# Performance work log

Hardware: AMD Instinct MI355X
Metric: run time of the kernel (lower is better)

The kernel has to match this reference:

```python
import jax, jax.numpy as jnp
import numpy as np
from jax import lax

ORDER = 6
WN = 0.5 / 50.0          # highpass_cutoff / (orig_fs/2)
UP, DOWN = 16, 25        # 64/100 reduced by gcd 4 (scipy resample_poly)
HALF_LEN = 10 * DOWN     # scipy kaiser half length = 10*max_rate
NTAPS = 2 * HALF_LEN + 1
PADLEN = 21              # sosfiltfilt default: 3*(2*n_sections+1), 3 biquads
CHANNELS = np.array([126, 125, 48, 112, 67, 93, 10, 61, 39, 108])
D_MODEL = 16
LN_EPS = 1e-5


def _butter_hp_sos(order, wn):
    # scipy.signal.butter(order, wn, btype='high', output='sos') in pure numpy
    fs = 2.0
    warped = 2.0 * fs * np.tan(np.pi * wn / fs)
    m = np.arange(-order + 1, order, 2)
    p = -np.exp(1j * np.pi * m / (2 * order))     # analog LP prototype poles
    k = np.real(1.0 / np.prod(-p))                # lp2hp gain (no zeros)
    p = warped / p                                # lp2hp poles; zeros at s=0
    z = np.zeros(order)
    fs2 = 2.0 * fs                                # bilinear, fs=2
    k = k * np.real(np.prod(fs2 - z) / np.prod(fs2 - p))
    z = (fs2 + z) / (fs2 - z)                     # digital zeros, all +1
    p = (fs2 + p) / (fs2 - p)
    pp = p[np.imag(p) > 0]
    pp = pp[np.argsort(-np.abs(np.abs(pp) - 1.0))]  # closest to unit circle last
    sos = []
    for i, pi in enumerate(pp):
        b = np.array([1.0, -2.0, 1.0]) * (k if i == 0 else 1.0)
        a = np.array([1.0, -2.0 * pi.real, np.abs(pi) ** 2])
        sos.append(np.concatenate([b, a]))
    return np.array(sos)


def _sosfilt_zi(sos):
    # scipy.signal.sosfilt_zi: steady-state of step response per section
    n = sos.shape[0]
    zi = np.zeros((n, 2))
    scale = 1.0
    for s in range(n):
        b0, b1, b2, _, a1, a2 = sos[s]
        A = np.array([[1.0 + a1, -1.0], [a2, 1.0]])
        B = np.array([b1 - a1 * b0, b2 - a2 * b0])
        zi[s] = scale * np.linalg.solve(A, B)
        scale *= (b0 + b1 + b2) / (1.0 + a1 + a2)
    return zi


SOS = _butter_hp_sos(ORDER, WN)
ZI = _sosfilt_zi(SOS)


def _resample_fir():
    # scipy firwin(2*half_len+1, 1/max_rate, window=('kaiser',5.0)) * up
    fc = 1.0 / DOWN
    m = np.arange(NTAPS) - (NTAPS - 1) / 2.0
    h = fc * np.sinc(fc * m) * np.kaiser(NTAPS, 5.0)
    h /= h.sum()
    return h * UP


H_BASE = _resample_fir()


def _pos_encoding(max_len, d):
    pos = np.arange(max_len)[:, None].astype(np.float64)
    div = np.exp(np.arange(0, d, 2) * (-np.log(10000.0) / d))
    pe = np.zeros((max_len, d))
    pe[:, 0::2] = np.sin(pos * div)
    pe[:, 1::2] = np.cos(pos * div)
    return pe.astype(np.float32)


PE = _pos_encoding(3840, D_MODEL)


def _sosfilt(x, zi):
    # x: (N,T), zi: (N,3,2). Cascade of biquads, transposed direct form II.
    sos = jnp.asarray(SOS, x.dtype)
    nsec = SOS.shape[0]

    def step(z, xt):
        v = xt
        zs = []
        for s in range(nsec):  # fixed tiny cascade, unrolled inside scan
            b0, b1, b2, a1, a2 = sos[s, 0], sos[s, 1], sos[s, 2], sos[s, 4], sos[s, 5]
            y = b0 * v + z[s][0]
            zs.append((b1 * v - a1 * y + z[s][1], b2 * v - a2 * y))
            v = y
        return tuple(zs), v

    z0 = tuple((zi[:, s, 0], zi[:, s, 1]) for s in range(nsec))
    _, y = lax.scan(step, z0, x.T)
    return y.T


def _sosfiltfilt(x):
    # scipy.signal.sosfiltfilt with default odd padding, padlen=21
    zi = jnp.asarray(ZI, x.dtype)
    front = 2.0 * x[:, :1] - x[:, PADLEN:0:-1]
    back = 2.0 * x[:, -1:] - x[:, -2:-PADLEN - 2:-1]
    ext = jnp.concatenate([front, x, back], axis=1)
    y = _sosfilt(ext, zi[None] * ext[:, 0, None, None])
    y = y[:, ::-1]
    y = _sosfilt(y, zi[None] * y[:, 0, None, None])
    return y[:, ::-1][:, PADLEN:-PADLEN]


def _resample_poly(x):
    # scipy.signal.resample_poly(x, 64, 100): upfirdn via dilated conv
    T = x.shape[-1]
    n_out = (T * UP) // DOWN + int((T * UP) % DOWN != 0)
    n_pre_pad = DOWN - HALF_LEN % DOWN
    n_pre_remove = (HALF_LEN + n_pre_pad) // DOWN

    def outlen(lh):
        return (((T - 1) * UP + lh) - 1) // DOWN + 1

    n_post = 0
    while outlen(NTAPS + n_pre_pad + n_post) < n_out + n_pre_remove:
        n_post += 1
    h = np.concatenate([np.zeros(n_pre_pad), H_BASE, np.zeros(n_post)])
    L = h.size
    rhs = jnp.asarray(h[::-1].copy(), x.dtype).reshape(1, 1, L)
    y = lax.conv_general_dilated(x[:, None, :], rhs, window_strides=(DOWN,),
                                 padding=[(L - 1, L - 1)], lhs_dilation=(UP,),
                                 dimension_numbers=('NCH', 'OIH', 'NCH'))
    return y[:, 0, n_pre_remove:n_pre_remove + n_out]


def _ln(x, g, b):
    mu = x.mean(-1, keepdims=True)
    var = ((x - mu) ** 2).mean(-1, keepdims=True)
    return (x - mu) * lax.rsqrt(var + LN_EPS) * g + b


def setup_inputs() -> dict:
    key = jax.random.key(0)
    ks = jax.random.split(key, 20)
    f32 = jnp.float32
    d = {
        'x': jax.random.normal(ks[0], (64, 128, 2000), f32),
        'conv_w': jax.random.normal(ks[1], (16, 10, 3), f32) * 0.15,
        'conv_b': jnp.zeros((16,), f32),
        'ln0_g': jnp.ones((16,), f32), 'ln0_b': jnp.zeros((16,), f32),
        'wqkv': jax.random.normal(ks[2], (48, 16), f32) * 0.125,
        'bqkv': jnp.zeros((48,), f32),
        'wo': jax.random.normal(ks[3], (16, 16), f32) * 0.25,
        'bo': jnp.zeros((16,), f32),
        'w1': jax.random.normal(ks[4], (32, 16), f32) * 0.2,
        'b1': jnp.zeros((32,), f32),
        'w2': jax.random.normal(ks[5], (16, 32), f32) * 0.2,
        'b2': jnp.zeros((16,), f32),
        'ln1_g': jnp.ones((16,), f32), 'ln1_b': jnp.zeros((16,), f32),
        'ln2_g': jnp.ones((16,), f32), 'ln2_b': jnp.zeros((16,), f32),
        'wfc': jax.random.normal(ks[6], (1, 16), f32) * 0.3,
        'bfc': jnp.zeros((1,), f32),
    }
    return d


def reference(x, conv_w, conv_b, ln0_g, ln0_b, wqkv, bqkv, wo, bo,
              w1, b1, w2, b2, ln1_g, ln1_b, ln2_g, ln2_b, wfc, bfc):
    B = x.shape[0]
    # remove Cz (last channel) then gather interesting channels
    x = x[:, :-1, :][:, jnp.asarray(CHANNELS), :]        # (B,10,T)
    x = x - x.mean(axis=1, keepdims=True)                # CAR
    C, T = x.shape[1], x.shape[2]
    xf = _sosfiltfilt(x.reshape(B * C, T))               # zero-phase highpass
    xr = _resample_poly(xf)                              # 100 Hz -> 64 Hz
    x = xr.reshape(B, C, -1)
    x = jnp.tanh(x)                                      # artifact_scale = 1.0
    mean = x.mean(axis=2, keepdims=True)                 # zscore, unbiased std
    var = ((x - mean) ** 2).sum(axis=2, keepdims=True) / (x.shape[2] - 1)
    std = jnp.maximum(jnp.sqrt(var), 1e-6)
    x = (x - mean) / std
    # conv1d k=3 pad=1 (10 -> 16) + relu
    x = lax.conv_general_dilated(x, conv_w, (1,), [(1, 1)],
                                 dimension_numbers=('NCH', 'OIH', 'NCH'))
    x = jax.nn.relu(x + conv_b[None, :, None])
    x = x.transpose(0, 2, 1)                             # (B,S,16)
    x = _ln(x, ln0_g, ln0_b)
    x = x + jnp.asarray(PE[:x.shape[1]], x.dtype)[None]
    # TransformerEncoderLayer, post-norm, nhead=1, relu FFN (eval: no dropout)
    qkv = x @ wqkv.T + bqkv
    q, k, v = jnp.split(qkv, 3, axis=-1)
    att = jax.nn.softmax(jnp.einsum('bqd,bkd->bqk', q, k) * 0.25, axis=-1)
    a = jnp.einsum('bqk,bkd->bqd', att, v) @ wo.T + bo
    x = _ln(x + a, ln1_g, ln1_b)
    f = jax.nn.relu(x @ w1.T + b1) @ w2.T + b2
    x = _ln(x + f, ln2_g, ln2_b)
    pooled = x.mean(axis=1)                              # adaptive avg pool -> 1
    return pooled @ wfc.T + bfc                          # (B,1)
```

## Files before the change

### kernel.cpp

```cpp
#include <hip/hip_runtime.h>
#include <cmath>
#include <complex>
#include <algorithm>

#ifndef M_PI
#define M_PI 3.14159265358979323846
#endif

typedef _Float16 f16x8 __attribute__((ext_vector_type(8)));
typedef _Float16 f16x4 __attribute__((ext_vector_type(4)));
typedef __fp16 fp16x2 __attribute__((ext_vector_type(2)));
typedef float f32x4 __attribute__((ext_vector_type(4)));

struct FiltArg {
  double b0[3], b1[3], b2[3], a1[3], a2[3];
  double zi0[3], zi1[3];
};
struct CorArg { double CA[16 * 6]; };
struct EigArg {
  double Pm[36], Pinv[36];
  double czi[6];
  double lam_re[3], lam_im[3];
  double lami_re[3], lami_im[3];
};
struct FirArg { float h[526]; };

static void design_sos(FiltArg& sa) {
  const int order = 6;
  const double wn = 0.5 / 50.0;
  const double fs = 2.0;
  double warped = 2.0 * fs * std::tan(M_PI * wn / fs);
  std::complex<double> p[6];
  for (int i = 0; i < order; i++) {
    int m = -order + 1 + 2 * i;
    p[i] = -std::exp(std::complex<double>(0.0, M_PI * m / (2.0 * order)));
  }
  std::complex<double> prod1(1, 0);
  for (int i = 0; i < 6; i++) prod1 *= -p[i];
  double k = (1.0 / prod1).real();
  for (int i = 0; i < 6; i++) p[i] = warped / p[i];
  const double fs2 = 2.0 * fs;
  std::complex<double> num(1, 0), den(1, 0);
  for (int i = 0; i < 6; i++) { num *= fs2; den *= (fs2 - p[i]); }
  k *= (num / den).real();
  for (int i = 0; i < 6; i++) p[i] = (fs2 + p[i]) / (fs2 - p[i]);
  std::complex<double> pp[3]; int n = 0;
  for (int i = 0; i < 6; i++) if (p[i].imag() > 0) pp[n++] = p[i];
  std::stable_sort(pp, pp + 3,
    [](const std::complex<double>& A, const std::complex<double>& B) {
      return std::fabs(std::abs(A) - 1.0) > std::fabs(std::abs(B) - 1.0);
    });
  double sos[3][6];
  for (int s = 0; s < 3; s++) {
    double g = (s == 0) ? k : 1.0;
    sos[s][0] = g; sos[s][1] = -2.0 * g; sos[s][2] = g;
    sos[s][3] = 1.0; sos[s][4] = -2.0 * pp[s].real(); sos[s][5] = std::norm(pp[s]);
  }
  double scale = 1.0;
  for (int s = 0; s < 3; s++) {
    double b0 = sos[s][0], b1 = sos[s][1], b2 = sos[s][2];
    double a1 = sos[s][4], a2 = sos[s][5];
    double det = 1.0 + a1 + a2;
    double r0 = b1 - a1 * b0, r1 = b2 - a2 * b0;
    double z0 = (r0 + r1) / det;
    double z1 = ((1.0 + a1) * r1 - a2 * r0) / det;
    sa.b0[s] = b0; sa.b1[s] = b1; sa.b2[s] = b2; sa.a1[s] = a1; sa.a2[s] = a2;
    sa.zi0[s] = scale * z0; sa.zi1[s] = scale * z1;
    scale *= (b0 + b1 + b2) / (1.0 + a1 + a2);
  }
}

static double host_step(const FiltArg& c, double z[6], double v) {
  for (int s = 0; s < 3; s++) {
    double y = c.b0[s] * v + z[2 * s];
    z[2 * s]     = c.b1[s] * v - c.a1[s] * y + z[2 * s + 1];
    z[2 * s + 1] = c.b2[s] * v - c.a2[s] * y;
    v = y;
  }
  return v;
}

static void build_filt(FiltArg& c, CorArg& co) {
  design_sos(c);
  for (int j = 0; j < 6; j++) {
    double z[6] = {0, 0, 0, 0, 0, 0};
    z[j] = 1.0;
    for (int i = 0; i < 16; i++) co.CA[i * 6 + j] = host_step(c, z, 0.0);
  }
}

static void build_eig(const FiltArg& c, EigArg& e) {
  double Pr[36];
  for (int s = 0; s < 3; s++) {
    double a1 = c.a1[s], a2 = c.a2[s];
    std::complex<double> disc = std::sqrt(std::complex<double>(a1 * a1 - 4.0 * a2, 0.0));
    std::complex<double> p = (-a1 + disc) / 2.0;
    if (p.imag() < 0) p = std::conj(p);
    std::complex<double> v[6] = {0, 0, 0, 0, 0, 0};
    v[2 * s] = 1.0;
    v[2 * s + 1] = a1 + p;
    std::complex<double> y = 1.0;
    for (int j = s + 1; j < 3; j++) {
      double b0j = c.b0[j], b1j = c.b1[j], b2j = c.b2[j];
      double a1j = c.a1[j], a2j = c.a2[j];
      std::complex<double> det = p * p + a1j * p + a2j;
      std::complex<double> r0 = (b1j - a1j * b0j) * y;
      std::complex<double> r1 = (b2j - a2j * b0j) * y;
      std::complex<double> z0 = (p * r0 + r1) / det;
      std::complex<double> z1 = ((p + a1j) * r1 - a2j * r0) / det;
      v[2 * j] = z0; v[2 * j + 1] = z1;
      y = b0j * y + z0;
    }
    for (int i = 0; i < 6; i++) {
      Pr[i * 6 + 2 * s]     = v[i].real();
      Pr[i * 6 + 2 * s + 1] = v[i].imag();
    }
    std::complex<double> lam = std::pow(p, 16);
    e.lam_re[s] = lam.real(); e.lam_im[s] = lam.imag();
    std::complex<double> li = 1.0 / lam;
    e.lami_re[s] = li.real(); e.lami_im[s] = li.imag();
  }
  for (int i = 0; i < 36; i++) e.Pm[i] = Pr[i];
  double M[6][12];
  for (int i = 0; i < 6; i++)
    for (int j = 0; j < 6; j++) { M[i][j] = Pr[i * 6 + j]; M[i][6 + j] = (i == j) ? 1.0 : 0.0; }
  for (int col = 0; col < 6; col++) {
    int piv = col;
    for (int i = col + 1; i < 6; i++)
      if (std::fabs(M[i][col]) > std::fabs(M[piv][col])) piv = i;
    if (piv != col) for (int j = 0; j < 12; j++) std::swap(M[col][j], M[piv][j]);
    double d = M[col][col];
    for (int j = 0; j < 12; j++) M[col][j] /= d;
    for (int i = 0; i < 6; i++) if (i != col) {
      double f = M[i][col];
      for (int j = 0; j < 12; j++) M[i][j] -= f * M[col][j];
    }
  }
  for (int i = 0; i < 6; i++)
    for (int j = 0; j < 6; j++) e.Pinv[i * 6 + j] = M[i][6 + j];
  double zv[6];
  for (int s = 0; s < 3; s++) { zv[2 * s] = c.zi0[s]; zv[2 * s + 1] = c.zi1[s]; }
  for (int i = 0; i < 6; i++) {
    double sum = 0.0;
    for (int j = 0; j < 6; j++) sum += e.Pinv[i * 6 + j] * zv[j];
    e.czi[i] = sum;
  }
}

static double bessel_i0(double x) {
  double s = 1.0, t = 1.0;
  for (int k = 1; k < 64; k++) {
    double u = x / (2.0 * k);
    t *= u * u; s += t;
    if (t < 1e-18 * s) break;
  }
  return s;
}

static void design_fir(FirArg& fa) {
  double h[501];
  const double fc = 1.0 / 25.0;
  double denom = bessel_i0(5.0);
  double sum = 0.0;
  for (int nn = 0; nn < 501; nn++) {
    double m = nn - 250.0;
    double xx = fc * m;
    double snc = (nn == 250) ? 1.0 : std::sin(M_PI * xx) / (M_PI * xx);
    double r = (2.0 * nn) / 500.0 - 1.0;
    double w = bessel_i0(5.0 * std::sqrt(std::max(0.0, 1.0 - r * r))) / denom;
    h[nn] = fc * snc * w; sum += h[nn];
  }
  for (int nn = 0; nn < 25; nn++) fa.h[nn] = 0.0f;
  for (int nn = 0; nn < 501; nn++) fa.h[25 + nn] = (float)(h[nn] / sum * 16.0);
}

__device__ inline double waveReduceSum(double v) {
  #pragma unroll
  for (int off = 32; off > 0; off >>= 1) v += __shfl_down(v, off, 64);
  return v;
}

__device__ inline void cpow_int(double br, double bi, int n, double& rr_, double& ri_) {
  double rr = 1.0, ri = 0.0;
  while (n) {
    if (n & 1) { double t = rr * br - ri * bi; ri = rr * bi + ri * br; rr = t; }
    double t2 = br * br - bi * bi; bi = 2.0 * br * bi; br = t2;
    n >>= 1;
  }
  rr_ = rr; ri_ = ri;
}

#define XR(t) xr[(t) + ((t) >> 5)]
#define YF(t) yf[(t) + ((t) >> 5)]
__global__ __launch_bounds__(128) void k_filt_resamp(const float* __restrict__ xin,
                                                     float* __restrict__ xn,
                                                     float* __restrict__ pe,
                                                     float* __restrict__ out,
                                                     FiltArg c, CorArg co, EigArg eg,
                                                     FirArg fa) {
  int bid = blockIdx.x;
  int gk = threadIdx.x;
  if (bid >= 640) {
    int i = (bid - 640) * 128 + gk;
    int t = i >> 4, d = i & 15, j2 = d >> 1;
    double div = exp(-((double)(2 * j2)) * 0.5756462732485114);
    double a = (double)t * div;
    pe[i] = (float)((d & 1) ? cos(a) : sin(a));
    if (bid == 799 && gk < 64) out[gk] = 0.f;
    return;
  }
  int r = (bid & 7) * 80 + (bid >> 3);
  __shared__ float xd[2000];
  __shared__ float xr[2112];
  __shared__ double yf[2112];
  __shared__ double wsum[3][2];
  __shared__ float hl[526];
  __shared__ double red[4];
  int lane = gk & 63;
  int wv = gk >> 6;
  int bb = r / 10, cc = r % 10;
  const int ch[10] = {126, 125, 48, 112, 67, 93, 10, 61, 39, 108};
  const float* xb = xin + (size_t)bb * 128 * 2000;

  for (int i = gk; i < 526; i += 128) hl[i] = fa.h[i];
  for (int t = gk; t < 2000; t += 128) {
    float own = 0.f, ssum = 0.f;
    #pragma unroll
    for (int c2 = 0; c2 < 10; c2++) {
      float vv = xb[ch[c2] * 2000 + t];
      ssum += vv;
      if (c2 == cc) own = vv;
    }
    xd[t] = own - ssum * 0.1f;
  }
  __syncthreads();

  float x0f = xd[0], xlf = xd[1999];
  for (int t = gk; t < 2048; t += 128) {
    float v;
    if (t < 21)        v = 2.f * x0f - xd[21 - t];
    else if (t < 2021) v = xd[t - 21];
    else if (t < 2042) v = 2.f * xlf - xd[4019 - t];
    else               v = 0.f;
    XR(t) = v;
  }
  __syncthreads();

  double b0[3], b1[3], b2[3], a1[3], a2[3];
  #pragma unroll
  for (int s = 0; s < 3; s++) {
    b0[s] = c.b0[s]; b1[s] = c.b1[s]; b2[s] = c.b2[s];
    a1[s] = c.a1[s]; a2[s] = c.a2[s];
  }
  auto step = [&](double* z, double v) -> double {
    #pragma unroll
    for (int s = 0; s < 3; s++) {
      double y = b0[s] * v + z[2 * s];
      z[2 * s]     = b1[s] * v - a1[s] * y + z[2 * s + 1];
      z[2 * s + 1] = b2[s] * v - a2[s] * y;
      v = y;
    }
    return v;
  };

  auto eigscan = [&](double seed, const double* F, double* zst) {
    double G[6];
    #pragma unroll
    for (int i = 0; i < 6; i++) {
      double s = 0.0;
      #pragma unroll
      for (int j = 0; j < 6; j++) s += eg.Pinv[i * 6 + j] * F[j];
      G[i] = s;
    }
    double tre[3], tim[3], sre[3], sim[3];
    #pragma unroll
    for (int s3 = 0; s3 < 3; s3++) {
      double gre = G[2 * s3], gim = -G[2 * s3 + 1];
      double mre, mim;
      cpow_int(eg.lami_re[s3], eg.lami_im[s3], gk, mre, mim);
      tre[s3] = mre * gre - mim * gim;
      tim[s3] = mre * gim + mim * gre;
      double pr = tre[s3], pi = tim[s3];
      #pragma unroll
      for (int off = 1; off < 64; off <<= 1) {
        double ore = __shfl_up(pr, off, 64);
        double oim = __shfl_up(pi, off, 64);
        pr += (lane >= off) ? ore : 0.0;
        pi += (lane >= off) ? oim : 0.0;
      }
      sre[s3] = pr; sim[s3] = pi;
      if (wv == 0 && lane == 63) { wsum[s3][0] = pr; wsum[s3][1] = pi; }
    }
    __syncthreads();
    double coord[6];
    #pragma unroll
    for (int s3 = 0; s3 < 3; s3++) {
      double inc_re = sre[s3] + (wv ? wsum[s3][0] : 0.0);
      double inc_im = sim[s3] + (wv ? wsum[s3][1] : 0.0);
      double Sre = inc_re - tre[s3], Sim = inc_im - tim[s3];
      double c0re = seed * eg.czi[2 * s3];
      double c0im = -seed * eg.czi[2 * s3 + 1];
      double lkre, lkim;
      cpow_int(eg.lam_re[s3], eg.lam_im[s3], gk, lkre, lkim);
      double lm1re = lkre * eg.lami_re[s3] - lkim * eg.lami_im[s3];
      double lm1im = lkre * eg.lami_im[s3] + lkim * eg.lami_re[s3];
      if (gk == 0) { lm1re = 0.0; lm1im = 0.0; }
      double cre = lkre * c0re - lkim * c0im + lm1re * Sre - lm1im * Sim;
      double cim = lkre * c0im + lkim * c0re + lm1re * Sim + lm1im * Sre;
      coord[2 * s3] = cre;
      coord[2 * s3 + 1] = -cim;
    }
    #pragma unroll
    for (int i = 0; i < 6; i++) {
      double s = 0.0;
      #pragma unroll
      for (int j = 0; j < 6; j++) s += eg.Pm[i * 6 + j] * coord[j];
      zst[i] = s;
    }
  };

  int t0 = gk * 16;
  double z[6], yreg[16], zst[6];

  #pragma unroll
  for (int i = 0; i < 6; i++) z[i] = 0.0;
  for (int i = 0; i < 16; i++) yreg[i] = step(z, (double)XR(t0 + i));
  eigscan((double)XR(0), z, zst);
  for (int i = 0; i < 16; i++) {
    double corr = 0.0;
    #pragma unroll
    for (int j = 0; j < 6; j++) corr += co.CA[i * 6 + j] * zst[j];
    YF(t0 + i) = yreg[i] + corr;
  }
  __syncthreads();

  auto rin = [&](int j) -> double { return (j <= 2041) ? YF(2041 - j) : 0.0; };
  double seedB = YF(2041);
  #pragma unroll
  for (int i = 0; i < 6; i++) z[i] = 0.0;
  for (int i = 0; i < 16; i++) yreg[i] = step(z, rin(t0 + i));
  eigscan(seedB, z, zst);
  for (int i = 0; i < 16; i++) {
    int j = t0 + i;
    if (j >= 21 && j <= 2020) {
      double corr = 0.0;
      #pragma unroll
      for (int jj = 0; jj < 6; jj++) corr += co.CA[i * 6 + jj] * zst[jj];
      xd[2020 - j] = (float)(yreg[i] + corr);
    }
  }
  __syncthreads();

  float vals[10];
  #pragma unroll
  for (int kk = 0; kk < 10; kk++) {
    int o = gk + kk * 128;
    int P = 25 * (o + 11);
    int phase = P & 15;
    float acc = 0.f;
    for (int m = phase; m <= 525; m += 16) {
      int idx = (P - m) >> 4;
      if (idx >= 0 && idx < 2000) acc += hl[m] * xd[idx];
    }
    vals[kk] = tanhf(acc);
  }
  double s = 0.0, ss = 0.0;
  #pragma unroll
  for (int kk = 0; kk < 10; kk++) {
    s += (double)vals[kk]; ss += (double)vals[kk] * (double)vals[kk];
  }
  s = waveReduceSum(s); ss = waveReduceSum(ss);
  if (lane == 0) { red[wv] = s; red[2 + wv] = ss; }
  __syncthreads();
  double S = red[0] + red[1];
  double SS = red[2] + red[3];
  double mean = S / 1280.0;
  double var = (SS - 1280.0 * mean * mean) / 1279.0;
  double sd = fmax(sqrt(fmax(var, 0.0)), 1e-6);
  float fmean = (float)mean, finv = (float)(1.0 / sd);
  #pragma unroll
  for (int kk = 0; kk < 10; kk++)
    xn[(size_t)r * 1280 + gk + kk * 128] = (vals[kk] - fmean) * finv;
}

__global__ __launch_bounds__(256) void k_conv_ln_pe_qkv(const float* __restrict__ xn,
    const float* __restrict__ cw, const float* __restrict__ cb,
    const float* __restrict__ g0, const float* __restrict__ bt0,
    const float* __restrict__ wqkv, const float* __restrict__ bqkv,
    const float* __restrict__ pe,
    float* __restrict__ x0, _Float16* __restrict__ Qh,
    _Float16* __restrict__ Kp, _Float16* __restrict__ Vt_g) {
  __shared__ float w[480], bias[16], gg[16], gb[16];
  __shared__ float wq[768], bq[48];
  for (int i = threadIdx.x; i < 480; i += 256) w[i] = cw[i];
  for (int i = threadIdx.x; i < 768; i += 256) wq[i] = wqkv[i];
  if (threadIdx.x < 16) {
    bias[threadIdx.x] = cb[threadIdx.x];
    gg[threadIdx.x] = g0[threadIdx.x];
    gb[threadIdx.x] = bt0[threadIdx.x];
  }
  if (threadIdx.x < 48) bq[threadIdx.x] = bqkv[threadIdx.x];
  __syncthreads();
  int idx = blockIdx.x * 256 + threadIdx.x;
  int b = idx / 1280, t = idx % 1280;
  const float* xb = xn + (size_t)b * 10 * 1280;
  float in[10][3];
  #pragma unroll
  for (int i = 0; i < 10; i++)
    #pragma unroll
    for (int k = 0; k < 3; k++) {
      int tt = t - 1 + k;
      in[i][k] = (tt >= 0 && tt < 1280) ? xb[i * 1280 + tt] : 0.f;
    }
  float o[16];
  #pragma unroll
  for (int oc = 0; oc < 16; oc++) {
    float a = bias[oc];
    #pragma unroll
    for (int i = 0; i < 10; i++)
      #pragma unroll
      for (int k = 0; k < 3; k++) a += in[i][k] * w[oc * 30 + i * 3 + k];
    o[oc] = fmaxf(a, 0.f);
  }
  float mu = 0.f;
  #pragma unroll
  for (int d = 0; d < 16; d++) mu += o[d];
  mu *= (1.f / 16.f);
  float var = 0.f;
  #pragma unroll
  for (int d = 0; d < 16; d++) { float dd = o[d] - mu; var += dd * dd; }
  var *= (1.f / 16.f);
  float inv = 1.f / sqrtf(var + 1e-5f);
  float xv[16];
  float* outp = x0 + (size_t)idx * 16;
  const float* pep = pe + t * 16;
  #pragma unroll
  for (int d = 0; d < 16; d++) {
    xv[d] = (o[d] - mu) * inv * gg[d] + gb[d] + pep[d];
    outp[d] = xv[d];
  }
  _Float16* qh = Qh + (size_t)idx * 16;
  #pragma unroll
  for (int j = 0; j < 16; j++) {
    float a = bq[j];
    #pragma unroll
    for (int d = 0; d < 16; d++) a += xv[d] * wq[j * 16 + d];
    qh[j] = (_Float16)(0.36067376f * a);
  }
  {
    _Float16* kp = Kp + (size_t)idx * 16;
    #pragma unroll
    for (int j = 0; j < 16; j++) {
      float a = bq[16 + j];
      #pragma unroll
      for (int d = 0; d < 16; d++) a += xv[d] * wq[(16 + j) * 16 + d];
      kp[j] = (_Float16)a;
    }
  }
  {
    _Float16* vt = Vt_g + (size_t)b * 16 * 1280 + t;
    #pragma unroll
    for (int j = 0; j < 16; j++) {
      float a = bq[32 + j];
      #pragma unroll
      for (int d = 0; d < 16; d++) a += xv[d] * wq[(32 + j) * 16 + d];
      vt[j * 1280] = (_Float16)a;
    }
  }
}

#define SHIFT2 17.3123404907f
__global__ __launch_bounds__(256) void k_attn_combine(const _Float16* __restrict__ Qh,
    const _Float16* __restrict__ Kp, const _Float16* __restrict__ Vt_g,
    const float* __restrict__ x0,
    const float* __restrict__ wo, const float* __restrict__ bo,
    const float* __restrict__ w1, const float* __restrict__ b1,
    const float* __restrict__ w2, const float* __restrict__ b2,
    const float* __restrict__ g1, const float* __restrict__ bb1,
    const float* __restrict__ g2, const float* __restrict__ bb2,
    const float* __restrict__ wfc, const float* __restrict__ bfc,
    float* __restrict__ out) {
  __shared__ __align__(16) _Float16 Ks[2][128 * 16];
  __shared__ __align__(16) _Float16 Vt[2][16 * 136];
  __shared__ float Aly[64][17];
  __shared__ float swo[256], sw1[512], sw2[512];
  __shared__ float sbo[16], sb1[32], sb2[16], sg1[16], sbb1[16], sg2[16], sbb2[16];
  __shared__ float swf[16];
  int tid = threadIdx.x;
  int bid = blockIdx.x;
  int jj  = bid >> 3;
  int b   = (bid & 7) + 8 * (jj & 7);
  int rg  = jj >> 3;
  int wv = tid >> 6;
  int lane = tid & 63;
  int col = lane & 15;
  int quad = lane >> 4;
  size_t base = (size_t)b * 1280;
  int row0 = rg * 64 + wv * 16;

  swo[tid] = wo[tid];
  for (int i = tid; i < 512; i += 256) { sw1[i] = w1[i]; sw2[i] = w2[i]; }
  if (tid < 16) {
    sbo[tid] = bo[tid]; sb2[tid] = b2[tid];
    sg1[tid] = g1[tid]; sbb1[tid] = bb1[tid];
    sg2[tid] = g2[tid]; sbb2[tid] = bb2[tid];
    swf[tid] = wfc[tid];
  }
  if (tid < 32) sb1[tid] = b1[tid];

  f16x8 qf;
  #pragma unroll
  for (int j = 0; j < 8; j++) qf[j] = (_Float16)0.f;
  if (quad < 2)
    qf = *(const f16x8*)(Qh + (base + row0 + col) * 16 + quad * 8);

  f16x8 ones;
  #pragma unroll
  for (int j = 0; j < 8; j++) ones[j] = (_Float16)1.f;

  const _Float16* kp_b = Kp + base * 16;
  const _Float16* vt_b = Vt_g + (size_t)b * 16 * 1280;

  int srow = tid >> 1, shalf = tid & 1;
  int sd = tid >> 4, sseg = tid & 15;

  {
    f16x8 kreg = *(const f16x8*)(kp_b + (size_t)srow * 16 + shalf * 8);
    f16x8 vreg = *(const f16x8*)(vt_b + (size_t)sd * 1280 + sseg * 8);
    *(f16x8*)&Ks[0][srow * 16 + shalf * 8] = kreg;
    *(f16x8*)&Vt[0][sd * 136 + sseg * 8] = vreg;
  }

  f32x4 oacc = {0.f, 0.f, 0.f, 0.f};
  f32x4 lacc = {0.f, 0.f, 0.f, 0.f};

  int sA = col + ((quad & 1) ? 32 : 0);
  int sB = sA + 16;
  bool hi = (quad >= 2);

  union U32H2 { fp16x2 h; unsigned int u; };
  union PFU { unsigned int u[4]; f16x8 v; };

  for (int s = 0; s < 10; s++) {
    int cur = s & 1;
    f16x8 kreg, vreg;
    if (s < 9) {
      kreg = *(const f16x8*)(kp_b + (size_t)((s + 1) * 128 + srow) * 16 + shalf * 8);
      vreg = *(const f16x8*)(vt_b + (size_t)sd * 1280 + (s + 1) * 128 + sseg * 8);
    }
    __syncthreads();
    const _Float16* ks = &Ks[cur][0];
    const _Float16* vt = &Vt[cur][0];

    unsigned int pp[8][2];
    #pragma unroll
    for (int st = 0; st < 8; st++) {
      f16x8 af;
      #pragma unroll
      for (int j = 0; j < 8; j++) af[j] = (_Float16)0.f;
      if (quad < 2)
        af = *(const f16x8*)&ks[(st * 16 + col) * 16 + quad * 8];
      f32x4 sf = {-SHIFT2, -SHIFT2, -SHIFT2, -SHIFT2};
      sf = __builtin_amdgcn_mfma_f32_16x16x32_f16(af, qf, sf, 0, 0, 0);
      float e0 = __builtin_amdgcn_exp2f(sf[0]);
      float e1 = __builtin_amdgcn_exp2f(sf[1]);
      float e2 = __builtin_amdgcn_exp2f(sf[2]);
      float e3 = __builtin_amdgcn_exp2f(sf[3]);
      U32H2 t0, t1;
      t0.h = __builtin_amdgcn_cvt_pkrtz(e0, e1);
      t1.h = __builtin_amdgcn_cvt_pkrtz(e2, e3);
      pp[st][0] = t0.u;
      pp[st][1] = t1.u;
    }

    #pragma unroll
    for (int c = 0; c < 4; c++) {
      int a00 = __shfl((int)pp[2 * c][0], sA, 64);
      int a01 = __shfl((int)pp[2 * c][1], sA, 64);
      int a10 = __shfl((int)pp[2 * c + 1][0], sA, 64);
      int a11 = __shfl((int)pp[2 * c + 1][1], sA, 64);
      int b00 = __shfl((int)pp[2 * c][0], sB, 64);
      int b01 = __shfl((int)pp[2 * c][1], sB, 64);
      int b10 = __shfl((int)pp[2 * c + 1][0], sB, 64);
      int b11 = __shfl((int)pp[2 * c + 1][1], sB, 64);
      PFU pu;
      pu.u[0] = (unsigned int)(hi ? a10 : a00);
      pu.u[1] = (unsigned int)(hi ? a11 : a01);
      pu.u[2] = (unsigned int)(hi ? b10 : b00);
      pu.u[3] = (unsigned int)(hi ? b11 : b01);
      f16x8 pf = pu.v;
      f16x8 vf = *(const f16x8*)&vt[col * 136 + c * 32 + quad * 8];
      oacc = __builtin_amdgcn_mfma_f32_16x16x32_f16(pf, vf, oacc, 0, 0, 0);
      lacc = __builtin_amdgcn_mfma_f32_16x16x32_f16(pf, ones, lacc, 0, 0, 0);
    }
    if (s < 9) {
      *(f16x8*)&Ks[cur ^ 1][srow * 16 + shalf * 8] = kreg;
      *(f16x8*)&Vt[cur ^ 1][sd * 136 + sseg * 8] = vreg;
    }
  }

  #pragma unroll
  for (int r = 0; r < 4; r++)
    Aly[wv * 16 + quad * 4 + r][col] = oacc[r] / lacc[r];
  __syncthreads();

  if (tid < 64) {
    int grow = rg * 64 + tid;
    size_t goff = (base + grow) * 16;
    float a[16];
    #pragma unroll
    for (int d = 0; d < 16; d++) a[d] = Aly[tid][d];
    float h[16];
    const float* xr = x0 + goff;
    #pragma unroll
    for (int d = 0; d < 16; d++) {
      float o = sbo[d];
      #pragma unroll
      for (int e = 0; e < 16; e++) o += a[e] * swo[d * 16 + e];
      h[d] = xr[d] + o;
    }
    float mu = 0.f;
    #pragma unroll
    for (int d = 0; d < 16; d++) mu += h[d];
    mu *= (1.f / 16.f);
    float var = 0.f;
    #pragma unroll
    for (int d = 0; d < 16; d++) { float dd = h[d] - mu; var += dd * dd; }
    var *= (1.f / 16.f);
    float inv = 1.f / sqrtf(var + 1e-5f);
    float x1[16];
    #pragma unroll
    for (int d = 0; d < 16; d++) x1[d] = (h[d] - mu) * inv * sg1[d] + sbb1[d];
    float t1[32];
    #pragma unroll
    for (int j = 0; j < 32; j++) {
      float u = sb1[j];
      #pragma unroll
      for (int d = 0; d < 16; d++) u += x1[d] * sw1[j * 16 + d];
      t1[j] = fmaxf(u, 0.f);
    }
    float h2[16];
    #pragma unroll
    for (int d = 0; d < 16; d++) {
      float u = sb2[d];
      #pragma unroll
      for (int j = 0; j < 32; j++) u += t1[j] * sw2[d * 32 + j];
      h2[d] = x1[d] + u;
    }
    mu = 0.f;
    #pragma unroll
    for (int d = 0; d < 16; d++) mu += h2[d];
    mu *= (1.f / 16.f);
    var = 0.f;
    #pragma unroll
    for (int d = 0; d < 16; d++) { float dd = h2[d] - mu; var += dd * dd; }
    var *= (1.f / 16.f);
    inv = 1.f / sqrtf(var + 1e-5f);
    float pv = 0.f;
    #pragma unroll
    for (int d = 0; d < 16; d++)
      pv += ((h2[d] - mu) * inv * sg2[d] + sbb2[d]) * swf[d];
    double part = waveReduceSum((double)pv);
    if (tid == 0) {
      float add = (float)(part / 1280.0);
      if (rg == 0) add += bfc[0];
      atomicAdd(&out[b], add);
    }
  }
}

extern "C" void kernel_launch(void* const* d_in, const int* in_sizes, int n_in,
                              void* d_out, int out_size, void* d_ws, size_t ws_size,
                              hipStream_t stream) {
  const float* x    = (const float*)d_in[0];
  const float* cw   = (const float*)d_in[1];
  const float* cb   = (const float*)d_in[2];
  const float* g0   = (const float*)d_in[3];
  const float* bt0  = (const float*)d_in[4];
  const float* wqkv = (const float*)d_in[5];
  const float* bqkv = (const float*)d_in[6];
  const float* wo   = (const float*)d_in[7];
  const float* bo   = (const float*)d_in[8];
  const float* w1   = (const float*)d_in[9];
  const float* b1   = (const float*)d_in[10];
  const float* w2   = (const float*)d_in[11];
  const float* b2   = (const float*)d_in[12];
  const float* g1   = (const float*)d_in[13];
  const float* bb1  = (const float*)d_in[14];
  const float* g2   = (const float*)d_in[15];
  const float* bb2  = (const float*)d_in[16];
  const float* wfc  = (const float*)d_in[17];
  const float* bfc  = (const float*)d_in[18];
  float* out = (float*)d_out;

  float* ws = (float*)d_ws;
  float* xs = ws;
  float* y1 = xs + 1280000;
  float* xn = y1 + 1306880;
  float* x0 = xn + 819200;
  _Float16* Qh   = (_Float16*)(x0 + 1310720);
  _Float16* Kp   = (_Float16*)(x0 + 1310720 + 655360);
  _Float16* Vt_g = (_Float16*)(x0 + 1310720 + 2 * 655360);
  float* pe = x0 + 1310720 + 3 * 655360;

  FiltArg fc; CorArg co; EigArg eg; FirArg fa;
  build_filt(fc, co);
  build_eig(fc, eg);
  design_fir(fa);

  k_filt_resamp<<<800, 128, 0, stream>>>(x, xn, pe, out, fc, co, eg, fa);
  k_conv_ln_pe_qkv<<<320, 256, 0, stream>>>(xn, cw, cb, g0, bt0, wqkv, bqkv,
                                            pe, x0, Qh, Kp, Vt_g);
  k_attn_combine<<<1280, 256, 0, stream>>>(Qh, Kp, Vt_g, x0, wo, bo, w1, b1,
                                           w2, b2, g1, bb1, g2, bb2, wfc, bfc,
                                           out);
}
```

Baseline: 235.8 us.

## Run the IIR filtfilt scan in fp32 with 256 threads and 8-sample chunks

Moves the biquad cascade, the eigen-decomposed parallel scan and the correction terms from double to float, and stores the intermediate forward-pass signal as float in shared memory. Each block now has 256 threads, each handling 8 samples instead of 16 (the eigenvalue power is updated to match). The cross-wave prefix sum now combines four waves, and the resample/zscore stage uses 5 outputs per thread. This aims to cut fp64 arithmetic and register pressure and to expose more parallelism per block. It risks accuracy loss, because a low-cutoff highpass with poles close to the unit circle is sensitive to single precision.

```diff
diff --git a/kernel.cpp b/kernel.cpp
--- a/kernel.cpp
+++ b/kernel.cpp
@@ -11,6 +11,8 @@
 typedef _Float16 f16x4 __attribute__((ext_vector_type(4)));
 typedef __fp16 fp16x2 __attribute__((ext_vector_type(2)));
 typedef float f32x4 __attribute__((ext_vector_type(4)));
+
+#define CHUNK 8
 
 struct FiltArg {
   double b0[3], b1[3], b2[3], a1[3], a2[3];
@@ -115,7 +117,7 @@
       Pr[i * 6 + 2 * s]     = v[i].real();
       Pr[i * 6 + 2 * s + 1] = v[i].imag();
     }
-    std::complex<double> lam = std::pow(p, 16);
+    std::complex<double> lam = std::pow(p, CHUNK);
     e.lam_re[s] = lam.real(); e.lam_im[s] = lam.imag();
     std::complex<double> li = 1.0 / lam;
     e.lami_re[s] = li.real(); e.lami_im[s] = li.imag();
@@ -180,19 +182,19 @@
   return v;
 }
 
-__device__ inline void cpow_int(double br, double bi, int n, double& rr_, double& ri_) {
-  double rr = 1.0, ri = 0.0;
+__device__ inline void cpowf_int(float br, float bi, int n, float& rr_, float& ri_) {
+  float rr = 1.f, ri = 0.f;
   while (n) {
-    if (n & 1) { double t = rr * br - ri * bi; ri = rr * bi + ri * br; rr = t; }
-    double t2 = br * br - bi * bi; bi = 2.0 * br * bi; br = t2;
+    if (n & 1) { float t = rr * br - ri * bi; ri = rr * bi + ri * br; rr = t; }
+    float t2 = br * br - bi * bi; bi = 2.f * br * bi; br = t2;
     n >>= 1;
   }
   rr_ = rr; ri_ = ri;
 }
 
 #define XR(t) xr[(t) + ((t) >> 5)]
-#define YF(t) yf[(t) + ((t) >> 5)]
-__global__ __launch_bounds__(128) void k_filt_resamp(const float* __restrict__ xin,
+#define YFS(t) yfs[(t) + ((t) >> 5)]
+__global__ __launch_bounds__(256) void k_filt_resamp(const float* __restrict__ xin,
                                                      float* __restrict__ xn,
                                                      float* __restrict__ pe,
                                                      float* __restrict__ out,
@@ -201,29 +203,29 @@
   int bid = blockIdx.x;
   int gk = threadIdx.x;
   if (bid >= 640) {
-    int i = (bid - 640) * 128 + gk;
+    int i = (bid - 640) * 256 + gk;
     int t = i >> 4, d = i & 15, j2 = d >> 1;
     double div = exp(-((double)(2 * j2)) * 0.5756462732485114);
     double a = (double)t * div;
     pe[i] = (float)((d & 1) ? cos(a) : sin(a));
-    if (bid == 799 && gk < 64) out[gk] = 0.f;
+    if (bid == 719 && gk < 64) out[gk] = 0.f;
     return;
   }
   int r = (bid & 7) * 80 + (bid >> 3);
   __shared__ float xd[2000];
-  __shared__ float xr[2112];
-  __shared__ double yf[2112];
-  __shared__ double wsum[3][2];
+  __shared__ float xr[2178];
+  __shared__ float yfs[2178];
   __shared__ float hl[526];
-  __shared__ double red[4];
+  __shared__ float wtot[3][4][2];
+  __shared__ double red[8];
   int lane = gk & 63;
   int wv = gk >> 6;
   int bb = r / 10, cc = r % 10;
   const int ch[10] = {126, 125, 48, 112, 67, 93, 10, 61, 39, 108};
   const float* xb = xin + (size_t)bb * 128 * 2000;
 
-  for (int i = gk; i < 526; i += 128) hl[i] = fa.h[i];
-  for (int t = gk; t < 2000; t += 128) {
+  for (int i = gk; i < 526; i += 256) hl[i] = fa.h[i];
+  for (int t = gk; t < 2000; t += 256) {
     float own = 0.f, ssum = 0.f;
     #pragma unroll
     for (int c2 = 0; c2 < 10; c2++) {
@@ -236,7 +238,7 @@
   __syncthreads();
 
   float x0f = xd[0], xlf = xd[1999];
-  for (int t = gk; t < 2048; t += 128) {
+  for (int t = gk; t < 2048; t += 256) {
     float v;
     if (t < 21)        v = 2.f * x0f - xd[21 - t];
     else if (t < 2021) v = xd[t - 21];
@@ -246,16 +248,16 @@
   }
   __syncthreads();
 
-  double b0[3], b1[3], b2[3], a1[3], a2[3];
+  float b0[3], b1[3], b2[3], a1[3], a2[3];
   #pragma unroll
   for (int s = 0; s < 3; s++) {
-    b0[s] = c.b0[s]; b1[s] = c.b1[s]; b2[s] = c.b2[s];
-    a1[s] = c.a1[s]; a2[s] = c.a2[s];
-  }
-  auto step = [&](double* z, double v) -> double {
+    b0[s] = (float)c.b0[s]; b1[s] = (float)c.b1[s]; b2[s] = (float)c.b2[s];
+    a1[s] = (float)c.a1[s]; a2[s] = (float)c.a2[s];
+  }
+  auto step = [&](float* z, float v) -> float {
     #pragma unroll
     for (int s = 0; s < 3; s++) {
-      double y = b0[s] * v + z[2 * s];
+      float y = b0[s] * v + z[2 * s];
       z[2 * s]     = b1[s] * v - a1[s] * y + z[2 * s + 1];
       z[2 * s + 1] = b2[s] * v - a2[s] * y;
       v = y;
@@ -263,98 +265,106 @@
     return v;
   };
 
-  auto eigscan = [&](double seed, const double* F, double* zst) {
-    double G[6];
+  auto eigscan = [&](float seed, const float* F, float* zst) {
+    float G[6];
     #pragma unroll
     for (int i = 0; i < 6; i++) {
-      double s = 0.0;
-      #pragma unroll
-      for (int j = 0; j < 6; j++) s += eg.Pinv[i * 6 + j] * F[j];
+      float s = 0.f;
+      #pragma unroll
+      for (int j = 0; j < 6; j++) s += (float)eg.Pinv[i * 6 + j] * F[j];
       G[i] = s;
     }
-    double tre[3], tim[3], sre[3], sim[3];
+    float tre[3], tim[3], sre[3], sim[3];
     #pragma unroll
     for (int s3 = 0; s3 < 3; s3++) {
-      double gre = G[2 * s3], gim = -G[2 * s3 + 1];
-      double mre, mim;
-      cpow_int(eg.lami_re[s3], eg.lami_im[s3], gk, mre, mim);
+      float gre = G[2 * s3], gim = -G[2 * s3 + 1];
+      float mre, mim;
+      cpowf_int((float)eg.lami_re[s3], (float)eg.lami_im[s3], gk, mre, mim);
       tre[s3] = mre * gre - mim * gim;
       tim[s3] = mre * gim + mim * gre;
-      double pr = tre[s3], pi = tim[s3];
+      float pr = tre[s3], pi = tim[s3];
       #pragma unroll
       for (int off = 1; off < 64; off <<= 1) {
-        double ore = __shfl_up(pr, off, 64);
-        double oim = __shfl_up(pi, off, 64);
-        pr += (lane >= off) ? ore : 0.0;
-        pi += (lane >= off) ? oim : 0.0;
+        float ore = __shfl_up(pr, off, 64);
+        float oim = __shfl_up(pi, off, 64);
+        pr += (lane >= off) ? ore : 0.f;
+        pi += (lane >= off) ? oim : 0.f;
       }
       sre[s3] = pr; sim[s3] = pi;
-      if (wv == 0 && lane == 63) { wsum[s3][0] = pr; wsum[s3][1] = pi; }
+      if (lane == 63) { wtot[s3][wv][0] = pr; wtot[s3][wv][1] = pi; }
     }
     __syncthreads();
-    double coord[6];
+    float coord[6];
     #pragma unroll
     for (int s3 = 0; s3 < 3; s3++) {
-      double inc_re = sre[s3] + (wv ? wsum[s3][0] : 0.0);
-      double inc_im = sim[s3] + (wv ? wsum[s3][1] : 0.0);
-      double Sre = inc_re - tre[s3], Sim = inc_im - tim[s3];
-      double c0re = seed * eg.czi[2 * s3];
-      double c0im = -seed * eg.czi[2 * s3 + 1];
-      double lkre, lkim;
-      cpow_int(eg.lam_re[s3], eg.lam_im[s3], gk, lkre, lkim);
-      double lm1re = lkre * eg.lami_re[s3] - lkim * eg.lami_im[s3];
-      double lm1im = lkre * eg.lami_im[s3] + lkim * eg.lami_re[s3];
-      if (gk == 0) { lm1re = 0.0; lm1im = 0.0; }
-      double cre = lkre * c0re - lkim * c0im + lm1re * Sre - lm1im * Sim;
-      double cim = lkre * c0im + lkim * c0re + lm1re * Sim + lm1im * Sre;
+      float inc_re = sre[s3], inc_im = sim[s3];
+      for (int w = 0; w < wv; w++) {
+        inc_re += wtot[s3][w][0];
+        inc_im += wtot[s3][w][1];
+      }
+      float Sre = inc_re - tre[s3], Sim = inc_im - tim[s3];
+      float c0re = seed * (float)eg.czi[2 * s3];
+      float c0im = -seed * (float)eg.czi[2 * s3 + 1];
+      float lkre, lkim;
+      cpowf_int((float)eg.lam_re[s3], (float)eg.lam_im[s3], gk, lkre, lkim);
+      float lamire = (float)eg.lami_re[s3], lamiim = (float)eg.lami_im[s3];
+      float lm1re = lkre * lamire - lkim * lamiim;
+      float lm1im = lkre * lamiim + lkim * lamire;
+      if (gk == 0) { lm1re = 0.f; lm1im = 0.f; }
+      float cre = lkre * c0re - lkim * c0im + lm1re * Sre - lm1im * Sim;
+      float cim = lkre * c0im + lkim * c0re + lm1re * Sim + lm1im * Sre;
       coord[2 * s3] = cre;
       coord[2 * s3 + 1] = -cim;
     }
     #pragma unroll
     for (int i = 0; i < 6; i++) {
-      double s = 0.0;
-      #pragma unroll
-      for (int j = 0; j < 6; j++) s += eg.Pm[i * 6 + j] * coord[j];
+      float s = 0.f;
+      #pragma unroll
+      for (int j = 0; j < 6; j++) s += (float)eg.Pm[i * 6 + j] * coord[j];
       zst[i] = s;
     }
   };
 
-  int t0 = gk * 16;
-  double z[6], yreg[16], zst[6];
-
-  #pragma unroll
-  for (int i = 0; i < 6; i++) z[i] = 0.0;
-  for (int i = 0; i < 16; i++) yreg[i] = step(z, (double)XR(t0 + i));
-  eigscan((double)XR(0), z, zst);
-  for (int i = 0; i < 16; i++) {
-    double corr = 0.0;
-    #pragma unroll
-    for (int j = 0; j < 6; j++) corr += co.CA[i * 6 + j] * zst[j];
-    YF(t0 + i) = yreg[i] + corr;
+  int t0 = gk * CHUNK;
+  float z[6], yreg[CHUNK], zst[6];
+
+  #pragma unroll
+  for (int i = 0; i < 6; i++) z[i] = 0.f;
+  #pragma unroll
+  for (int i = 0; i < CHUNK; i++) yreg[i] = step(z, XR(t0 + i));
+  eigscan(XR(0), z, zst);
+  #pragma unroll
+  for (int i = 0; i < CHUNK; i++) {
+    float corr = 0.f;
+    #pragma unroll
+    for (int j = 0; j < 6; j++) corr += (float)co.CA[i * 6 + j] * zst[j];
+    YFS(t0 + i) = yreg[i] + corr;
   }
   __syncthreads();
 
-  auto rin = [&](int j) -> double { return (j <= 2041) ? YF(2041 - j) : 0.0; };
-  double seedB = YF(2041);
-  #pragma unroll
-  for (int i = 0; i < 6; i++) z[i] = 0.0;
-  for (int i = 0; i < 16; i++) yreg[i] = step(z, rin(t0 + i));
+  auto rin = [&](int j) -> float { return (j <= 2041) ? YFS(2041 - j) : 0.f; };
+  float seedB = YFS(2041);
+  #pragma unroll
+  for (int i = 0; i < 6; i++) z[i] = 0.f;
+  #pragma unroll
+  for (int i = 0; i < CHUNK; i++) yreg[i] = step(z, rin(t0 + i));
   eigscan(seedB, z, zst);
-  for (int i = 0; i < 16; i++) {
+  #pragma unroll
+  for (int i = 0; i < CHUNK; i++) {
     int j = t0 + i;
     if (j >= 21 && j <= 2020) {
-      double corr = 0.0;
-      #pragma unroll
-      for (int jj = 0; jj < 6; jj++) corr += co.CA[i * 6 + jj] * zst[jj];
-      xd[2020 - j] = (float)(yreg[i] + corr);
+      float corr = 0.f;
+      #pragma unroll
+      for (int jj = 0; jj < 6; jj++) corr += (float)co.CA[i * 6 + jj] * zst[jj];
+      xd[2020 - j] = yreg[i] + corr;
     }
   }
   __syncthreads();
 
-  float vals[10];
-  #pragma unroll
-  for (int kk = 0; kk < 10; kk++) {
-    int o = gk + kk * 128;
+  float vals[5];
+  #pragma unroll
+  for (int kk = 0; kk < 5; kk++) {
+    int o = gk + kk * 256;
     int P = 25 * (o + 11);
     int phase = P & 15;
     float acc = 0.f;
@@ -366,21 +376,21 @@
   }
   double s = 0.0, ss = 0.0;
   #pragma unroll
-  for (int kk = 0; kk < 10; kk++) {
+  for (int kk = 0; kk < 5; kk++) {
     s += (double)vals[kk]; ss += (double)vals[kk] * (double)vals[kk];
   }
   s = waveReduceSum(s); ss = waveReduceSum(ss);
-  if (lane == 0) { red[wv] = s; red[2 + wv] = ss; }
+  if (lane == 0) { red[wv] = s; red[4 + wv] = ss; }
   __syncthreads();
-  double S = red[0] + red[1];
-  double SS = red[2] + red[3];
+  double S = red[0] + red[1] + red[2] + red[3];
+  double SS = red[4] + red[5] + red[6] + red[7];
   double mean = S / 1280.0;
   double var = (SS - 1280.0 * mean * mean) / 1279.0;
   double sd = fmax(sqrt(fmax(var, 0.0)), 1e-6);
   float fmean = (float)mean, finv = (float)(1.0 / sd);
   #pragma unroll
-  for (int kk = 0; kk < 10; kk++)
-    xn[(size_t)r * 1280 + gk + kk * 128] = (vals[kk] - fmean) * finv;
+  for (int kk = 0; kk < 5; kk++)
+    xn[(size_t)r * 1280 + gk + kk * 256] = (vals[kk] - fmean) * finv;
 }
 
 __global__ __launch_bounds__(256) void k_conv_ln_pe_qkv(const float* __restrict__ xn,
@@ -708,7 +718,7 @@
   build_eig(fc, eg);
   design_fir(fa);
 
-  k_filt_resamp<<<800, 128, 0, stream>>>(x, xn, pe, out, fc, co, eg, fa);
+  k_filt_resamp<<<720, 256, 0, stream>>>(x, xn, pe, out, fc, co, eg, fa);
   k_conv_ln_pe_qkv<<<320, 256, 0, stream>>>(xn, cw, cb, g0, bt0, wqkv, bqkv,
                                             pe, x0, Qh, Kp, Vt_g);
   k_attn_combine<<<1280, 256, 0, stream>>>(Qh, Kp, Vt_g, x0, wo, bo, w1, b1,
```

Result: faster. 215.9 us (-8.4%).
